# Optimization experiments

Measured on AMD Instinct MI355X. Metric: run time of the kernel, lower is better.

## Reference

```python
import jax, jax.numpy as jnp
import numpy as np

B, H, M, DH = 8, 32, 8, 64  # batch, spatial h=w, heads, dim_head
C = M * DH
HW = H * H


def _make_pos_idx(h: int) -> np.ndarray:
    # A[i, j] = j - i, matching tf.constant([range(i, i+h) for i in range(0, -h, -1)])
    A = np.arange(h)[None, :] - np.arange(h)[:, None]
    horiz = np.tile(A, (h, h))                              # (h^2, h^2)
    vert = np.repeat(np.repeat(A, h, axis=0), h, axis=1)    # (h^2, h^2)
    return (2 * h - 1) * (vert + h - 1) + (horiz + h - 1)   # values in [0, (2h-1)^2)


def setup_inputs() -> dict:
    key = jax.random.key(0)
    ks = jax.random.split(key, 4)
    x = jax.random.normal(ks[0], (B, H, H, C), dtype=jnp.float32)
    w_qkv = jax.random.normal(ks[1], (DH, 3 * DH), dtype=jnp.float32) * (1.0 / np.sqrt(DH))
    b_qkv = jnp.zeros((3 * DH,), dtype=jnp.float32)
    w_ht = jax.random.normal(ks[2], (C, C), dtype=jnp.float32) * (1.0 / np.sqrt(C))
    b_ht = jnp.zeros((C,), dtype=jnp.float32)
    # Glorot-normal scalar table over (2h-1)^2 relative positions
    n_rel = (2 * H - 1) ** 2
    pos_table = jax.random.normal(ks[3], (n_rel,), dtype=jnp.float32) * np.float32(np.sqrt(2.0 / (n_rel + 1)))
    pos_idx = jnp.asarray(_make_pos_idx(H), dtype=jnp.int32)  # (HW, HW)
    return {"x": x, "w_qkv": w_qkv, "b_qkv": b_qkv, "w_ht": w_ht, "b_ht": b_ht,
            "pos_table": pos_table, "pos_idx": pos_idx}


def reference(x, w_qkv, b_qkv, w_ht, b_ht, pos_table, pos_idx):
    b, h, w, c = x.shape
    d_h = c // M
    # split heads into the batch dim: (b*M, h, w, d_h)
    xh = x.reshape(b, h, w, M, d_h).transpose(0, 3, 1, 2, 4).reshape(b * M, h, w, d_h)
    # 1x1 conv == per-pixel dense
    qkv = xh @ w_qkv + b_qkv                       # (b*M, h, w, 3*DH)
    qkv = qkv.reshape(b * M, h * w, DH, 3)
    q, k, v = qkv[..., 0], qkv[..., 1], qkv[..., 2]
    q = q / jnp.sqrt(jnp.float32(DH))
    att = jnp.einsum('bic,bjc->bij', q, k)         # (b*M, HW, HW)
    pos_emb = pos_table[pos_idx]                   # (HW, HW) gathered bias
    att = jax.nn.softmax(att + pos_emb, axis=-1)
    o = jnp.einsum('bij,bjc->bic', att, v)         # (b*M, HW, DH)
    o = o.reshape(b, M, h, w, d_h).transpose(0, 2, 3, 1, 4).reshape(b, h, w, c)
    out = o @ w_ht + b_ht                          # 1x1 head_transform conv
    return (out, att, pos_emb)
```

## Files before the change

kernel.cpp:

```cpp
#include <hip/hip_runtime.h>
#include <hip/hip_bf16.h>

typedef __attribute__((ext_vector_type(8))) __bf16 bf16x8;
typedef __attribute__((ext_vector_type(8))) short  s16x8;
typedef __attribute__((ext_vector_type(4))) short  s16x4;
typedef __attribute__((ext_vector_type(4))) float  f32x4;

#define HW2 1024
#define CDIM 512

static __device__ __forceinline__ unsigned short f2b(float f) {
  __hip_bfloat16 h = __float2bfloat16(f);
  return __builtin_bit_cast(unsigned short, h);
}

static __device__ __forceinline__ f32x4 mfma16(s16x8 a, s16x8 b, f32x4 c) {
  return __builtin_amdgcn_mfma_f32_16x16x32_bf16(
      __builtin_bit_cast(bf16x8, a), __builtin_bit_cast(bf16x8, b), c, 0, 0, 0);
}

__global__ __launch_bounds__(256) void k_prep(
    const float* __restrict__ w_qkv, const float* __restrict__ w_ht,
    const float* __restrict__ table, const int* __restrict__ idx,
    unsigned short* __restrict__ Wtq, unsigned short* __restrict__ Wtk,
    unsigned short* __restrict__ Wtv, unsigned short* __restrict__ WhtT,
    float* __restrict__ pe) {
  int blk = blockIdx.x;
  if (blk < 16) {
    int i = blk * 256 + threadIdx.x;
    int c = i >> 6, k = i & 63;
    const float* src = w_qkv + k * 192 + 3 * c;
    Wtq[i] = f2b(src[0] * 0.125f);
    Wtk[i] = f2b(src[1]);
    Wtv[i] = f2b(src[2]);
  } else if (blk < 1040) {
    int i = (blk - 16) * 256 + threadIdx.x;
    int c = i >> 9, k = i & 511;
    WhtT[i] = f2b(w_ht[k * 512 + c]);
  } else {
    int i = (blk - 1040) * 256 + threadIdx.x;
    #pragma unroll
    for (int j = 0; j < 4; ++j) {
      int p = i + j * 262144;
      pe[p] = table[idx[p]];
    }
  }
}

__global__ __launch_bounds__(256) void k_qkv(const float* __restrict__ x,
    const float* __restrict__ b_qkv,
    const unsigned short* __restrict__ Wtq, const unsigned short* __restrict__ Wtk,
    const unsigned short* __restrict__ Wtv,
    unsigned short* __restrict__ Qb, unsigned short* __restrict__ Kb,
    unsigned short* __restrict__ Vt) {
  int bm = blockIdx.x >> 4;
  int pt = blockIdx.x & 15;
  int wid = threadIdx.x >> 6, lane = threadIdx.x & 63;
  int l15 = lane & 15, lg = lane >> 4;
  int b = bm >> 3, m = bm & 7;
  int pbase = pt * 64 + wid * 16;

  int pA = pbase + l15;
  const float* xp = x + (size_t)(b * HW2 + pA) * CDIM + m * 64 + lg * 8;
  f32x4 xv0 = *(const f32x4*)(xp);
  f32x4 xv1 = *(const f32x4*)(xp + 4);
  f32x4 xv2 = *(const f32x4*)(xp + 32);
  f32x4 xv3 = *(const f32x4*)(xp + 36);
  s16x8 a0, a1;
  #pragma unroll
  for (int j = 0; j < 4; ++j) {
    a0[j]     = (short)f2b(xv0[j]);
    a0[4 + j] = (short)f2b(xv1[j]);
    a1[j]     = (short)f2b(xv2[j]);
    a1[4 + j] = (short)f2b(xv3[j]);
  }

  f32x4 acc[12];
  #pragma unroll
  for (int ct = 0; ct < 12; ++ct) acc[ct] = (f32x4){0.f, 0.f, 0.f, 0.f};

  #pragma unroll
  for (int ct = 0; ct < 12; ++ct) {
    const unsigned short* W = (ct < 4) ? Wtq : (ct < 8 ? Wtk : Wtv);
    int c = (ct & 3) * 16 + l15;
    const unsigned short* wp = W + c * 64 + lg * 8;
    s16x8 b0 = *(const s16x8*)(wp);
    s16x8 b1 = *(const s16x8*)(wp + 32);
    if (ct < 8) {
      acc[ct] = mfma16(b0, a0, acc[ct]);
      acc[ct] = mfma16(b1, a1, acc[ct]);
    } else {
      acc[ct] = mfma16(a0, b0, acc[ct]);
      acc[ct] = mfma16(a1, b1, acc[ct]);
    }
  }

  #pragma unroll
  for (int ct = 0; ct < 8; ++ct) {
    int s = ct >> 2;
    int c0 = (ct & 3) * 16 + lg * 4;
    unsigned short* D = (s == 0) ? Qb : Kb;
    s16x4 pk;
    #pragma unroll
    for (int i = 0; i < 4; ++i) {
      float bias = b_qkv[3 * (c0 + i) + s];
      if (s == 0) bias *= 0.125f;
      pk[i] = (short)f2b(acc[ct][i] + bias);
    }
    *(s16x4*)(D + (size_t)(bm * HW2 + pbase + l15) * 64 + c0) = pk;
  }
  #pragma unroll
  for (int ct = 8; ct < 12; ++ct) {
    int c = (ct & 3) * 16 + l15;
    float bias = b_qkv[3 * c + 2];
    s16x4 pk;
    #pragma unroll
    for (int i = 0; i < 4; ++i) pk[i] = (short)f2b(acc[ct][i] + bias);
    *(s16x4*)(Vt + ((size_t)bm * 64 + c) * HW2 + pbase + lg * 4) = pk;
  }
}

__global__ __launch_bounds__(256, 4) void k_attn(
    const unsigned short* __restrict__ Qb, const unsigned short* __restrict__ Kb,
    const unsigned short* __restrict__ Vt, const float* __restrict__ ptab,
    float* __restrict__ att, unsigned short* __restrict__ O) {
  int r8 = blockIdx.x & 7;
  int kk = blockIdx.x >> 3;
  int qt = kk & 63;
  int bm = ((kk >> 6) << 3) | r8;
  int wid = threadIdx.x >> 6, lane = threadIdx.x & 63;
  int l15 = lane & 15, lg = lane >> 4;

  __shared__ unsigned short P[16][1032];
  __shared__ float redm[4][16];
  __shared__ float reds[4][16];

  const unsigned short* qp = Qb + (size_t)(bm * HW2 + qt * 16 + l15) * 64 + lg * 8;
  s16x8 qa0 = *(const s16x8*)qp;
  s16x8 qa1 = *(const s16x8*)(qp + 32);

  f32x4 acc[16];
  const unsigned short* kbase = Kb + (size_t)bm * HW2 * 64;
  #pragma unroll
  for (int ct = 0; ct < 16; ++ct) {
    int col = wid * 256 + ct * 16 + l15;
    const unsigned short* kp = kbase + (size_t)col * 64 + lg * 8;
    s16x8 kb0 = *(const s16x8*)kp;
    s16x8 kb1 = *(const s16x8*)(kp + 32);
    f32x4 a = (f32x4){0.f, 0.f, 0.f, 0.f};
    a = mfma16(kb0, qa0, a);
    a = mfma16(kb1, qa1, a);
    acc[ct] = a;
  }

  int cb = 1984 - 63 * (qt >> 1) - ((qt & 1) << 4) - l15;
  float pm = -1e30f;
  #pragma unroll
  for (int ct = 0; ct < 16; ++ct) {
    int c0 = wid * 256 + ct * 16 + lg * 4;
    int t0 = 63 * (c0 >> 5) + (c0 & 31) + cb;
    f32x4 pv;
    __builtin_memcpy(&pv, ptab + t0, 16);
    #pragma unroll
    for (int i = 0; i < 4; ++i) {
      float v = acc[ct][i] + pv[i];
      acc[ct][i] = v;
      pm = fmaxf(pm, v);
    }
  }
  pm = fmaxf(pm, __shfl_xor(pm, 16));
  pm = fmaxf(pm, __shfl_xor(pm, 32));

  float ps = 0.f;
  #pragma unroll
  for (int ct = 0; ct < 16; ++ct) {
    #pragma unroll
    for (int i = 0; i < 4; ++i) {
      float e = __expf(acc[ct][i] - pm);
      acc[ct][i] = e;
      ps += e;
    }
  }
  ps += __shfl_xor(ps, 16);
  ps += __shfl_xor(ps, 32);
  if (lane < 16) { redm[wid][l15] = pm; reds[wid][l15] = ps; }
  __syncthreads();

  float m0 = redm[0][l15], m1 = redm[1][l15];
  float m2 = redm[2][l15], m3 = redm[3][l15];
  float m = fmaxf(fmaxf(m0, m1), fmaxf(m2, m3));
  float denom = reds[0][l15] * __expf(m0 - m) + reds[1][l15] * __expf(m1 - m)
              + reds[2][l15] * __expf(m2 - m) + reds[3][l15] * __expf(m3 - m);
  float scale = __expf(pm - m) / denom;

  #pragma unroll
  for (int ct = 0; ct < 16; ++ct) {
    int c0 = wid * 256 + ct * 16 + lg * 4;
    s16x4 pk;
    #pragma unroll
    for (int i = 0; i < 4; ++i) {
      float v = acc[ct][i] * scale;
      acc[ct][i] = v;
      pk[i] = (short)f2b(v);
    }
    *(s16x4*)&P[l15][c0] = pk;
  }
  __syncthreads();

  f32x4 o = (f32x4){0.f, 0.f, 0.f, 0.f};
  const unsigned short* vbase = Vt + (size_t)(bm * 64 + wid * 16 + l15) * HW2;
  #pragma unroll
  for (int kt = 0; kt < 32; ++kt) {
    s16x8 vb = *(const s16x8*)(vbase + kt * 32 + lg * 8);
    s16x8 pa = *(const s16x8*)&P[l15][kt * 32 + lg * 8];
    o = mfma16(vb, pa, o);
  }
  s16x4 ok;
  #pragma unroll
  for (int i = 0; i < 4; ++i) ok[i] = (short)f2b(o[i]);
  *(s16x4*)(O + (size_t)(bm * HW2 + qt * 16 + l15) * 64 + wid * 16 + lg * 4) = ok;

  float* abase = att + (size_t)(bm * HW2 + qt * 16 + l15) * HW2;
  #pragma unroll
  for (int ct = 0; ct < 16; ++ct) {
    int c0 = wid * 256 + ct * 16 + lg * 4;
    f32x4 vv;
    #pragma unroll
    for (int i = 0; i < 4; ++i) vv[i] = acc[ct][i];
    __builtin_nontemporal_store(vv, (f32x4*)(abase + c0));
  }
}

__global__ __launch_bounds__(256) void k_ht(
    const unsigned short* __restrict__ O, const unsigned short* __restrict__ WhtT,
    const float* __restrict__ b_ht, float* __restrict__ out) {
  int rt = blockIdx.x >> 1;
  int ch = blockIdx.x & 1;
  int wid = threadIdx.x >> 6, lane = threadIdx.x & 63;
  int wr = wid >> 1, wc = wid & 1;
  int l15 = lane & 15, lg = lane >> 4;
  int b = (rt * 32) >> 10;
  int p0 = (rt * 32) & 1023;

  __shared__ unsigned short A[32][520];

  int t = threadIdx.x;
  #pragma unroll
  for (int j = 0; j < 8; ++j) {
    int idx = t * 8 + j * 2048;
    int row = idx >> 9;
    int k0 = idx & 511;
    int m = k0 >> 6, kk = k0 & 63;
    const unsigned short* src = O + (size_t)((b * 8 + m) * HW2 + p0 + row) * 64 + kk;
    *(s16x8*)&A[row][k0] = *(const s16x8*)src;
  }
  __syncthreads();

  f32x4 acc[8];
  #pragma unroll
  for (int ct = 0; ct < 8; ++ct) acc[ct] = (f32x4){0.f, 0.f, 0.f, 0.f};

  #pragma unroll
  for (int kt = 0; kt < 16; ++kt) {
    s16x8 a = *(const s16x8*)&A[wr * 16 + l15][kt * 32 + lg * 8];
    #pragma unroll
    for (int ct = 0; ct < 8; ++ct) {
      int col = ch * 256 + wc * 128 + ct * 16 + l15;
      s16x8 bf = *(const s16x8*)(WhtT + (size_t)col * 512 + kt * 32 + lg * 8);
      acc[ct] = mfma16(bf, a, acc[ct]);
    }
  }

  int rp = rt * 32 + wr * 16 + l15;
  #pragma unroll
  for (int ct = 0; ct < 8; ++ct) {
    int c0 = ch * 256 + wc * 128 + ct * 16 + lg * 4;
    f32x4 bb = *(const f32x4*)(b_ht + c0);
    f32x4 ov;
    #pragma unroll
    for (int i = 0; i < 4; ++i) ov[i] = acc[ct][i] + bb[i];
    *(f32x4*)(out + (size_t)rp * 512 + c0) = ov;
  }
}

extern "C" void kernel_launch(void* const* d_in, const int* in_sizes, int n_in,
                              void* d_out, int out_size, void* d_ws, size_t ws_size,
                              hipStream_t stream) {
  const float* x         = (const float*)d_in[0];
  const float* w_qkv     = (const float*)d_in[1];
  const float* b_qkv     = (const float*)d_in[2];
  const float* w_ht      = (const float*)d_in[3];
  const float* b_ht      = (const float*)d_in[4];
  const float* pos_table = (const float*)d_in[5];
  const int*   pos_idx   = (const int*)d_in[6];

  float* out = (float*)d_out;
  float* att = out + 4194304;
  float* pe  = att + 67108864;

  char* ws = (char*)d_ws;
  unsigned short* Qb   = (unsigned short*)(ws);
  unsigned short* Kb   = (unsigned short*)(ws + (8u  << 20));
  unsigned short* Vt   = (unsigned short*)(ws + (16u << 20));
  unsigned short* O    = (unsigned short*)(ws + (24u << 20));
  unsigned short* Wtq  = (unsigned short*)(ws + (32u << 20));
  unsigned short* Wtk  = Wtq + 4096;
  unsigned short* Wtv  = Wtk + 4096;
  unsigned short* WhtT = (unsigned short*)(ws + (32u << 20) + 65536);

  k_prep<<<2064, 256, 0, stream>>>(w_qkv, w_ht, pos_table, pos_idx,
                                   Wtq, Wtk, Wtv, WhtT, pe);
  k_qkv <<<1024, 256, 0, stream>>>(x, b_qkv, Wtq, Wtk, Wtv, Qb, Kb, Vt);
  k_attn<<<4096, 256, 0, stream>>>(Qb, Kb, Vt, pos_table, att, O);
  k_ht  <<<512,  256, 0, stream>>>(O, WhtT, b_ht, out);
}
```

Measured before the change: 220.9 us.

## Warp-specialize attention kernel with LDS-staged coalesced att stores overlapping compute

The attention kernel now uses 512-thread blocks that each handle 8 query tiles in sequence. Four waves compute QK^T, softmax and PV, writing the normalized probabilities into a swizzled fp32 LDS staging buffer. The other four waves stream the previous tile's probabilities to global memory as full contiguous row stores. The goal is to overlap the large att output write with the next tile's compute and to make those stores better coalesced. In exchange, the large LDS footprint limits the kernel to one block per CU, and half the waves do no math, so latency hiding depends on the pipelining working.

After: 254.6 us. 15.3% more time.

```diff
diff --git a/kernel.cpp b/kernel.cpp
--- a/kernel.cpp
+++ b/kernel.cpp
@@ -17,6 +17,13 @@
 static __device__ __forceinline__ f32x4 mfma16(s16x8 a, s16x8 b, f32x4 c) {
   return __builtin_amdgcn_mfma_f32_16x16x32_bf16(
       __builtin_bit_cast(bf16x8, a), __builtin_bit_cast(bf16x8, b), c, 0, 0, 0);
+}
+
+static __device__ __forceinline__ void bar_lgkm() {
+  __builtin_amdgcn_sched_barrier(0);
+  asm volatile("s_waitcnt lgkmcnt(0)" ::: "memory");
+  __builtin_amdgcn_s_barrier();
+  __builtin_amdgcn_sched_barrier(0);
 }
 
 __global__ __launch_bounds__(256) void k_prep(
@@ -120,114 +127,153 @@
   }
 }
 
-__global__ __launch_bounds__(256, 4) void k_attn(
+__global__ __launch_bounds__(512, 1) void k_attn(
     const unsigned short* __restrict__ Qb, const unsigned short* __restrict__ Kb,
     const unsigned short* __restrict__ Vt, const float* __restrict__ ptab,
     float* __restrict__ att, unsigned short* __restrict__ O) {
   int r8 = blockIdx.x & 7;
-  int kk = blockIdx.x >> 3;
-  int qt = kk & 63;
-  int bm = ((kk >> 6) << 3) | r8;
+  int g  = (blockIdx.x >> 3) & 7;
+  int bm = ((blockIdx.x >> 6) << 3) | r8;
   int wid = threadIdx.x >> 6, lane = threadIdx.x & 63;
   int l15 = lane & 15, lg = lane >> 4;
-
+  int w4 = wid & 3;
+  bool writer = wid >= 4;
+
+  __shared__ __align__(16) float stg[16][1024];
   __shared__ unsigned short P[16][1032];
   __shared__ float redm[4][16];
   __shared__ float reds[4][16];
 
-  const unsigned short* qp = Qb + (size_t)(bm * HW2 + qt * 16 + l15) * 64 + lg * 8;
-  s16x8 qa0 = *(const s16x8*)qp;
-  s16x8 qa1 = *(const s16x8*)(qp + 32);
-
-  f32x4 acc[16];
   const unsigned short* kbase = Kb + (size_t)bm * HW2 * 64;
-  #pragma unroll
-  for (int ct = 0; ct < 16; ++ct) {
-    int col = wid * 256 + ct * 16 + l15;
-    const unsigned short* kp = kbase + (size_t)col * 64 + lg * 8;
-    s16x8 kb0 = *(const s16x8*)kp;
-    s16x8 kb1 = *(const s16x8*)(kp + 32);
-    f32x4 a = (f32x4){0.f, 0.f, 0.f, 0.f};
-    a = mfma16(kb0, qa0, a);
-    a = mfma16(kb1, qa1, a);
-    acc[ct] = a;
-  }
-
-  int cb = 1984 - 63 * (qt >> 1) - ((qt & 1) << 4) - l15;
-  float pm = -1e30f;
-  #pragma unroll
-  for (int ct = 0; ct < 16; ++ct) {
-    int c0 = wid * 256 + ct * 16 + lg * 4;
-    int t0 = 63 * (c0 >> 5) + (c0 & 31) + cb;
-    f32x4 pv;
-    __builtin_memcpy(&pv, ptab + t0, 16);
-    #pragma unroll
-    for (int i = 0; i < 4; ++i) {
-      float v = acc[ct][i] + pv[i];
-      acc[ct][i] = v;
-      pm = fmaxf(pm, v);
-    }
-  }
-  pm = fmaxf(pm, __shfl_xor(pm, 16));
-  pm = fmaxf(pm, __shfl_xor(pm, 32));
-
-  float ps = 0.f;
-  #pragma unroll
-  for (int ct = 0; ct < 16; ++ct) {
-    #pragma unroll
-    for (int i = 0; i < 4; ++i) {
-      float e = __expf(acc[ct][i] - pm);
-      acc[ct][i] = e;
-      ps += e;
-    }
-  }
-  ps += __shfl_xor(ps, 16);
-  ps += __shfl_xor(ps, 32);
-  if (lane < 16) { redm[wid][l15] = pm; reds[wid][l15] = ps; }
-  __syncthreads();
-
-  float m0 = redm[0][l15], m1 = redm[1][l15];
-  float m2 = redm[2][l15], m3 = redm[3][l15];
-  float m = fmaxf(fmaxf(m0, m1), fmaxf(m2, m3));
-  float denom = reds[0][l15] * __expf(m0 - m) + reds[1][l15] * __expf(m1 - m)
-              + reds[2][l15] * __expf(m2 - m) + reds[3][l15] * __expf(m3 - m);
-  float scale = __expf(pm - m) / denom;
-
-  #pragma unroll
-  for (int ct = 0; ct < 16; ++ct) {
-    int c0 = wid * 256 + ct * 16 + lg * 4;
-    s16x4 pk;
-    #pragma unroll
-    for (int i = 0; i < 4; ++i) {
-      float v = acc[ct][i] * scale;
-      acc[ct][i] = v;
-      pk[i] = (short)f2b(v);
-    }
-    *(s16x4*)&P[l15][c0] = pk;
-  }
-  __syncthreads();
-
-  f32x4 o = (f32x4){0.f, 0.f, 0.f, 0.f};
-  const unsigned short* vbase = Vt + (size_t)(bm * 64 + wid * 16 + l15) * HW2;
-  #pragma unroll
-  for (int kt = 0; kt < 32; ++kt) {
-    s16x8 vb = *(const s16x8*)(vbase + kt * 32 + lg * 8);
-    s16x8 pa = *(const s16x8*)&P[l15][kt * 32 + lg * 8];
-    o = mfma16(vb, pa, o);
-  }
-  s16x4 ok;
-  #pragma unroll
-  for (int i = 0; i < 4; ++i) ok[i] = (short)f2b(o[i]);
-  *(s16x4*)(O + (size_t)(bm * HW2 + qt * 16 + l15) * 64 + wid * 16 + lg * 4) = ok;
-
-  float* abase = att + (size_t)(bm * HW2 + qt * 16 + l15) * HW2;
-  #pragma unroll
-  for (int ct = 0; ct < 16; ++ct) {
-    int c0 = wid * 256 + ct * 16 + lg * 4;
-    f32x4 vv;
-    #pragma unroll
-    for (int i = 0; i < 4; ++i) vv[i] = acc[ct][i];
-    __builtin_nontemporal_store(vv, (f32x4*)(abase + c0));
+
+  #pragma unroll 1
+  for (int t = 0; t < 8; ++t) {
+    int qt = g * 8 + t;
+    f32x4 acc[16];
+    float pm = -1e30f;
+
+    if (!writer) {
+      const unsigned short* qp =
+          Qb + (size_t)(bm * HW2 + qt * 16 + l15) * 64 + lg * 8;
+      s16x8 qa0 = *(const s16x8*)qp;
+      s16x8 qa1 = *(const s16x8*)(qp + 32);
+      #pragma unroll
+      for (int ct = 0; ct < 16; ++ct) {
+        int col = w4 * 256 + ct * 16 + l15;
+        const unsigned short* kp = kbase + (size_t)col * 64 + lg * 8;
+        s16x8 kb0 = *(const s16x8*)kp;
+        s16x8 kb1 = *(const s16x8*)(kp + 32);
+        f32x4 a = (f32x4){0.f, 0.f, 0.f, 0.f};
+        a = mfma16(kb0, qa0, a);
+        a = mfma16(kb1, qa1, a);
+        acc[ct] = a;
+      }
+      int cb = 1984 - 63 * (qt >> 1) - ((qt & 1) << 4) - l15;
+      #pragma unroll
+      for (int ct = 0; ct < 16; ++ct) {
+        int c0 = w4 * 256 + ct * 16 + lg * 4;
+        int t0 = 63 * (c0 >> 5) + (c0 & 31) + cb;
+        f32x4 pv;
+        __builtin_memcpy(&pv, ptab + t0, 16);
+        #pragma unroll
+        for (int i = 0; i < 4; ++i) {
+          float v = acc[ct][i] + pv[i];
+          acc[ct][i] = v;
+          pm = fmaxf(pm, v);
+        }
+      }
+      pm = fmaxf(pm, __shfl_xor(pm, 16));
+      pm = fmaxf(pm, __shfl_xor(pm, 32));
+      float ps = 0.f;
+      #pragma unroll
+      for (int ct = 0; ct < 16; ++ct) {
+        #pragma unroll
+        for (int i = 0; i < 4; ++i) {
+          float e = __expf(acc[ct][i] - pm);
+          acc[ct][i] = e;
+          ps += e;
+        }
+      }
+      ps += __shfl_xor(ps, 16);
+      ps += __shfl_xor(ps, 32);
+      if (lane < 16) { redm[w4][l15] = pm; reds[w4][l15] = ps; }
+    } else if (t > 0) {
+      int qtt = g * 8 + t - 1;
+      float* ab = att + (size_t)(bm * HW2 + qtt * 16) * HW2;
+      #pragma unroll
+      for (int rr = 0; rr < 4; ++rr) {
+        int r = w4 * 4 + rr;
+        #pragma unroll
+        for (int j = 0; j < 4; ++j) {
+          int chunk = j * 64 + lane;
+          int sw = chunk ^ (r & 7);
+          f32x4 v = *(const f32x4*)&stg[r][sw * 4];
+          __builtin_nontemporal_store(v,
+              (f32x4*)(ab + (size_t)r * HW2 + chunk * 4));
+        }
+      }
+    }
+    bar_lgkm();
+
+    if (!writer) {
+      float m = redm[0][l15];
+      #pragma unroll
+      for (int w = 1; w < 4; ++w) m = fmaxf(m, redm[w][l15]);
+      float denom = 0.f;
+      #pragma unroll
+      for (int w = 0; w < 4; ++w)
+        denom += reds[w][l15] * __expf(redm[w][l15] - m);
+      float scale = __expf(pm - m) / denom;
+      #pragma unroll
+      for (int ct = 0; ct < 16; ++ct) {
+        f32x4 vv;
+        s16x4 pk;
+        #pragma unroll
+        for (int i = 0; i < 4; ++i) {
+          float v = acc[ct][i] * scale;
+          vv[i] = v;
+          pk[i] = (short)f2b(v);
+        }
+        int chunk = w4 * 64 + ct * 4 + lg;
+        *(f32x4*)&stg[l15][(chunk ^ (l15 & 7)) * 4] = vv;
+        *(s16x4*)&P[l15][w4 * 256 + ct * 16 + lg * 4] = pk;
+      }
+    }
+    bar_lgkm();
+
+    if (!writer) {
+      f32x4 o = (f32x4){0.f, 0.f, 0.f, 0.f};
+      const unsigned short* vbase =
+          Vt + (size_t)(bm * 64 + w4 * 16 + l15) * HW2;
+      #pragma unroll
+      for (int kt = 0; kt < 32; ++kt) {
+        s16x8 vb = *(const s16x8*)(vbase + kt * 32 + lg * 8);
+        s16x8 pa = *(const s16x8*)&P[l15][kt * 32 + lg * 8];
+        o = mfma16(vb, pa, o);
+      }
+      s16x4 ok;
+      #pragma unroll
+      for (int i = 0; i < 4; ++i) ok[i] = (short)f2b(o[i]);
+      *(s16x4*)(O + (size_t)(bm * HW2 + qt * 16 + l15) * 64 +
+                w4 * 16 + lg * 4) = ok;
+    }
+  }
+
+  if (writer) {
+    int qtt = g * 8 + 7;
+    float* ab = att + (size_t)(bm * HW2 + qtt * 16) * HW2;
+    #pragma unroll
+    for (int rr = 0; rr < 4; ++rr) {
+      int r = w4 * 4 + rr;
+      #pragma unroll
+      for (int j = 0; j < 4; ++j) {
+        int chunk = j * 64 + lane;
+        int sw = chunk ^ (r & 7);
+        f32x4 v = *(const f32x4*)&stg[r][sw * 4];
+        __builtin_nontemporal_store(v,
+            (f32x4*)(ab + (size_t)r * HW2 + chunk * 4));
+      }
+    }
   }
 }
 
@@ -311,6 +357,6 @@
   k_prep<<<2064, 256, 0, stream>>>(w_qkv, w_ht, pos_table, pos_idx,
                                    Wtq, Wtk, Wtv, WhtT, pe);
   k_qkv <<<1024, 256, 0, stream>>>(x, b_qkv, Wtq, Wtk, Wtv, Qb, Kb, Vt);
-  k_attn<<<4096, 256, 0, stream>>>(Qb, Kb, Vt, pos_table, att, O);
+  k_attn<<<512,  512, 0, stream>>>(Qb, Kb, Vt, pos_table, att, O);
   k_ht  <<<512,  256, 0, stream>>>(O, WhtT, b_ht, out);
 }
```
